# Kernel optimization log

Measured on AMD Instinct MI355X. Metric: run time of the kernel, lower is better.

## Reference

```python
import jax, jax.numpy as jnp
import numpy as np

B, L, D, H = 4, 2048, 256, 8
HD = D // H

def setup_inputs() -> dict:
    key = jax.random.key(0)
    ks = jax.random.split(key, 11)
    s = 1.0 / np.sqrt(D)
    return {
        "key": jax.random.normal(ks[0], (B, L, D), jnp.float32),
        "value": jax.random.normal(ks[1], (B, L, D), jnp.float32),
        "query": jax.random.normal(ks[2], (B, L, D), jnp.float32),
        "Wk": jax.random.normal(ks[3], (D, D), jnp.float32) * s,
        "bk": jnp.zeros((D,), jnp.float32),
        "Wq": jax.random.normal(ks[4], (D, D), jnp.float32) * s,
        "bq": jnp.zeros((D,), jnp.float32),
        "Wv": jax.random.normal(ks[5], (D, D), jnp.float32) * s,
        "bv": jnp.zeros((D,), jnp.float32),
        "Wp": jax.random.normal(ks[6], (D, D), jnp.float32) * s,
        "bp": jnp.zeros((D,), jnp.float32),
    }

def reference(key, value, query, Wk, bk, Wq, bq, Wv, bv, Wp, bp):
    # torch Linear: x @ W.T + b
    k = (key @ Wk.T + bk).reshape(B, L, H, HD).transpose(0, 2, 1, 3)   # [B,H,L,HD]
    q = (query @ Wq.T + bq).reshape(B, L, H, HD).transpose(0, 2, 1, 3)
    v = (value @ Wv.T + bv).reshape(B, L, H, HD).transpose(0, 2, 1, 3)
    att = jnp.einsum('bhqd,bhkd->bhqk', q, k) * (1.0 / np.sqrt(HD))    # [B,H,L,L]
    # causal mask (tril)
    causal = jnp.tril(jnp.ones((L, L), bool))
    att = jnp.where(causal[None, None], att, -jnp.inf)
    att = jax.nn.softmax(att, axis=-1)
    y = jnp.einsum('bhqk,bhkd->bhqd', att, v)                          # [B,H,L,HD]
    y = y.transpose(0, 2, 1, 3).reshape(B, L, D)
    return y @ Wp.T + bp
```

## Files before the change

kernel.cpp:

```cpp
#include <hip/hip_runtime.h>
#include <hip/hip_bf16.h>
#include <cstdint>

#define BB 4
#define LL 2048
#define DD 256
#define HH 8
#define HDIM 32
#define MTOT (BB * LL)
#define BHT (BB * HH)
#define XS (MTOT * DD)
#define WSZ (DD * DD)

typedef __attribute__((ext_vector_type(8))) short short8;
typedef __attribute__((ext_vector_type(4))) float f32x4;

static constexpr float SCALE = 0.17677669529663687f;
static constexpr float FMAX = 8.0f;

__device__ __forceinline__ unsigned f2bf(float f) {
    const unsigned u = __builtin_bit_cast(unsigned, f);
    return (u + 0x7fffu + ((u >> 16) & 1u)) >> 16;
}
__device__ __forceinline__ float bf2f(unsigned h) {
    return __builtin_bit_cast(float, h << 16);
}

__device__ __forceinline__ void split_store(const float4 f, unsigned short* hb,
                                            unsigned short* lb, size_t base) {
    const float fv[4] = {f.x, f.y, f.z, f.w};
    unsigned h[4], l[4];
#pragma unroll
    for (int j = 0; j < 4; ++j) {
        h[j] = f2bf(fv[j]);
        l[j] = f2bf(fv[j] - bf2f(h[j]));
    }
    *(uint2*)&hb[base] = make_uint2(h[0] | (h[1] << 16), h[2] | (h[3] << 16));
    *(uint2*)&lb[base] = make_uint2(l[0] | (l[1] << 16), l[2] | (l[3] << 16));
}

__global__ __launch_bounds__(256) void prep_x(const float* __restrict__ s0,
                                              const float* __restrict__ s1,
                                              const float* __restrict__ s2,
                                              unsigned short* __restrict__ xh,
                                              unsigned short* __restrict__ xl) {
    const int t = blockIdx.y;
    const float* src = (t == 0) ? s0 : (t == 1 ? s1 : s2);
    const size_t i4 = (size_t)blockIdx.x * 256 + threadIdx.x;
    const float4 f = ((const float4*)src)[i4];
    split_store(f, xh, xl, (size_t)t * XS + i4 * 4);
}

__global__ __launch_bounds__(256) void prep_w(const float* __restrict__ w0,
                                              const float* __restrict__ w1,
                                              const float* __restrict__ w2,
                                              const float* __restrict__ w3,
                                              unsigned short* __restrict__ wh,
                                              unsigned short* __restrict__ wl) {
    const int t = blockIdx.y;
    const float* src = (t == 0) ? w0 : (t == 1 ? w1 : (t == 2 ? w2 : w3));
    const size_t i4 = (size_t)blockIdx.x * 256 + threadIdx.x;
    const float4 f = ((const float4*)src)[i4];
    split_store(f, wh, wl, (size_t)t * WSZ + i4 * 4);
}

template <int MODE>
__global__ __launch_bounds__(256) void gemm_bf16x2(const unsigned short* __restrict__ Ah,
                                                   const unsigned short* __restrict__ Al,
                                                   const unsigned short* __restrict__ Wh,
                                                   const unsigned short* __restrict__ Wl,
                                                   const float* __restrict__ bias,
                                                   void* __restrict__ Cout) {
    const int tid = threadIdx.x;
    const int w = tid >> 6;
    const int lane = tid & 63;
    const int g = lane >> 4;
    const int c = lane & 15;
    const int bm = blockIdx.x * 64;
    const int bn = blockIdx.y * 64;
    const int m0w = bm + w * 16;

    f32x4 acc[4] = {};

    const unsigned short* arow_h = Ah + (size_t)(m0w + c) * DD + 8 * g;
    const unsigned short* arow_l = Al + (size_t)(m0w + c) * DD + 8 * g;

#pragma unroll
    for (int k0 = 0; k0 < DD; k0 += 32) {
        const short8 ah = *(const short8*)(arow_h + k0);
        const short8 al = *(const short8*)(arow_l + k0);
#pragma unroll
        for (int nf = 0; nf < 4; ++nf) {
            const size_t woff = (size_t)(bn + nf * 16 + c) * DD + k0 + 8 * g;
            const short8 wh = *(const short8*)(Wh + woff);
            const short8 wl = *(const short8*)(Wl + woff);
            acc[nf] = __builtin_amdgcn_mfma_f32_16x16x32_bf16(ah, wh, acc[nf], 0, 0, 0);
            acc[nf] = __builtin_amdgcn_mfma_f32_16x16x32_bf16(ah, wl, acc[nf], 0, 0, 0);
            acc[nf] = __builtin_amdgcn_mfma_f32_16x16x32_bf16(al, wh, acc[nf], 0, 0, 0);
        }
    }

#pragma unroll
    for (int nf = 0; nf < 4; ++nf) {
        const int n = bn + nf * 16 + c;
        const float bj = bias[n];
        if constexpr (MODE == 0) {
            float* C = (float*)Cout;
#pragma unroll
            for (int r = 0; r < 4; ++r)
                C[(size_t)(m0w + 4 * g + r) * DD + n] = acc[nf][r] + bj;
        } else if constexpr (MODE == 1 || MODE == 2) {
            unsigned short* C = (unsigned short*)Cout;
            const int h_ = n >> 5, d_ = n & 31;
#pragma unroll
            for (int r = 0; r < 4; ++r) {
                const int m = m0w + 4 * g + r;
                const int b_ = m >> 11, l_ = m & (LL - 1);
                float v = acc[nf][r] + bj;
                if (MODE == 1) v *= SCALE;
                C[(((size_t)b_ * HH + h_) * LL + l_) * HDIM + d_] = (unsigned short)f2bf(v);
            }
        } else {
            unsigned short* C = (unsigned short*)Cout;
            const int h_ = n >> 5, d_ = n & 31;
            const int m = m0w + 4 * g;
            const int b_ = m >> 11, l_ = m & (LL - 1);
            const unsigned lo = f2bf(acc[nf][0] + bj) | (f2bf(acc[nf][1] + bj) << 16);
            const unsigned hi = f2bf(acc[nf][2] + bj) | (f2bf(acc[nf][3] + bj) << 16);
            *(uint2*)&C[(((size_t)b_ * HH + h_) * HDIM + d_) * LL + l_] = make_uint2(lo, hi);
        }
    }
}

__global__ __launch_bounds__(256) void attn_mfma(const unsigned short* __restrict__ qb,
                                                 const unsigned short* __restrict__ kb,
                                                 const unsigned short* __restrict__ vt,
                                                 unsigned short* __restrict__ yh,
                                                 unsigned short* __restrict__ yl) {
    __shared__ unsigned short plds[4][16][66];
    const int tid = threadIdx.x;
    const int w = tid >> 6;
    const int lane = tid & 63;
    const int g = lane >> 4;
    const int c = lane & 15;
    const int qblk = (int)(gridDim.x - 1 - blockIdx.x);
    const int bh = blockIdx.y;
    const int qrow0 = qblk * 64 + w * 16;

    const unsigned short* Qp = qb + (size_t)bh * LL * HDIM;
    const unsigned short* Kp = kb + (size_t)bh * LL * HDIM;
    const unsigned short* Vp = vt + (size_t)bh * HDIM * LL;

    const short8 qf = *(const short8*)(Qp + (size_t)(qrow0 + c) * HDIM + g * 8);

    f32x4 y0 = {0.f, 0.f, 0.f, 0.f};
    f32x4 y1 = {0.f, 0.f, 0.f, 0.f};
    float lsum = 0.f;

    auto step = [&](int kt, bool masked) {
        const f32x4 z = {0.f, 0.f, 0.f, 0.f};
        f32x4 st[4];
#pragma unroll
        for (int t = 0; t < 4; ++t) {
            const short8 kf = *(const short8*)(Kp + (size_t)(kt + 16 * t + c) * HDIM + g * 8);
            st[t] = __builtin_amdgcn_mfma_f32_16x16x32_bf16(kf, qf, z, 0, 0, 0);
        }
        if (masked) {
#pragma unroll
            for (int t = 0; t < 4; ++t)
#pragma unroll
                for (int r = 0; r < 4; ++r)
                    if (kt + 16 * t + 4 * g + r > qrow0 + c) st[t][r] = -1e30f;
        }
#pragma unroll
        for (int t = 0; t < 4; ++t) {
            const float p0 = __expf(st[t][0] - FMAX);
            const float p1 = __expf(st[t][1] - FMAX);
            const float p2 = __expf(st[t][2] - FMAX);
            const float p3 = __expf(st[t][3] - FMAX);
            lsum += (p0 + p1) + (p2 + p3);
            const unsigned lo = f2bf(p0) | (f2bf(p1) << 16);
            const unsigned hi = f2bf(p2) | (f2bf(p3) << 16);
            *(uint2*)&plds[w][c][16 * t + 4 * g] = make_uint2(lo, hi);
        }
        asm volatile("s_waitcnt lgkmcnt(0)" ::: "memory");
        __builtin_amdgcn_sched_barrier(0);
        const unsigned short* prow = &plds[w][c][0];
        const short8 pa0 = *(const short8*)(prow + g * 8);
        const short8 pa1 = *(const short8*)(prow + 32 + g * 8);
        const short8 v00 = *(const short8*)(Vp + (size_t)c * LL + kt + g * 8);
        const short8 v10 = *(const short8*)(Vp + (size_t)c * LL + kt + 32 + g * 8);
        const short8 v01 = *(const short8*)(Vp + (size_t)(16 + c) * LL + kt + g * 8);
        const short8 v11 = *(const short8*)(Vp + (size_t)(16 + c) * LL + kt + 32 + g * 8);
        y0 = __builtin_amdgcn_mfma_f32_16x16x32_bf16(pa0, v00, y0, 0, 0, 0);
        y0 = __builtin_amdgcn_mfma_f32_16x16x32_bf16(pa1, v10, y0, 0, 0, 0);
        y1 = __builtin_amdgcn_mfma_f32_16x16x32_bf16(pa0, v01, y1, 0, 0, 0);
        y1 = __builtin_amdgcn_mfma_f32_16x16x32_bf16(pa1, v11, y1, 0, 0, 0);
    };

    for (int kt = 0; kt < qblk * 64; kt += 64) step(kt, false);
    step(qblk * 64, true);

    lsum += __shfl_xor(lsum, 16);
    lsum += __shfl_xor(lsum, 32);
#pragma unroll
    for (int r = 0; r < 4; ++r) {
        const float ls = __shfl(lsum, (lane & 48) | (4 * g + r));
        const float inv = 1.f / ls;
        const size_t base =
            ((size_t)(bh >> 3) * LL + qrow0 + 4 * g + r) * DD + (bh & 7) * HDIM;
        const float v0 = y0[r] * inv;
        const float v1 = y1[r] * inv;
        const unsigned h0 = f2bf(v0), h1 = f2bf(v1);
        yh[base + c] = (unsigned short)h0;
        yl[base + c] = (unsigned short)f2bf(v0 - bf2f(h0));
        yh[base + 16 + c] = (unsigned short)h1;
        yl[base + 16 + c] = (unsigned short)f2bf(v1 - bf2f(h1));
    }
}

extern "C" void kernel_launch(void* const* d_in, const int* in_sizes, int n_in,
                              void* d_out, int out_size, void* d_ws, size_t ws_size,
                              hipStream_t stream) {
    const float* key   = (const float*)d_in[0];
    const float* value = (const float*)d_in[1];
    const float* query = (const float*)d_in[2];
    const float* Wk = (const float*)d_in[3];
    const float* bk = (const float*)d_in[4];
    const float* Wq = (const float*)d_in[5];
    const float* bq = (const float*)d_in[6];
    const float* Wv = (const float*)d_in[7];
    const float* bv = (const float*)d_in[8];
    const float* Wp = (const float*)d_in[9];
    const float* bp = (const float*)d_in[10];
    float* out = (float*)d_out;

    unsigned short* xh = (unsigned short*)d_ws;
    unsigned short* xl = xh + (size_t)3 * XS;
    unsigned short* wh = xl + (size_t)3 * XS;
    unsigned short* wl = wh + (size_t)4 * WSZ;
    unsigned short* qb = wl + (size_t)4 * WSZ;
    unsigned short* kb = qb + XS;
    unsigned short* vt = kb + XS;
    unsigned short* yh = vt + XS;
    unsigned short* yl = yh + XS;

    prep_x<<<dim3(2048, 3), 256, 0, stream>>>(key, value, query, xh, xl);
    prep_w<<<dim3(64, 4), 256, 0, stream>>>(Wk, Wq, Wv, Wp, wh, wl);

    const unsigned short* kxh = xh, *vxh = xh + XS, *qxh = xh + 2 * (size_t)XS;
    const unsigned short* kxl = xl, *vxl = xl + XS, *qxl = xl + 2 * (size_t)XS;

    const dim3 gg(MTOT / 64, DD / 64);
    gemm_bf16x2<1><<<gg, 256, 0, stream>>>(qxh, qxl, wh + WSZ, wl + WSZ, bq, qb);
    gemm_bf16x2<2><<<gg, 256, 0, stream>>>(kxh, kxl, wh, wl, bk, kb);
    gemm_bf16x2<3><<<gg, 256, 0, stream>>>(vxh, vxl, wh + 2 * (size_t)WSZ,
                                           wl + 2 * (size_t)WSZ, bv, vt);
    attn_mfma<<<dim3(LL / 64, BHT), 256, 0, stream>>>(qb, kb, vt, yh, yl);
    gemm_bf16x2<0><<<gg, 256, 0, stream>>>(yh, yl, wh + 3 * (size_t)WSZ,
                                           wl + 3 * (size_t)WSZ, bp, out);
}
```

Before: 260.4 us.

## Merge QKV projections into one launch, halve GEMM N-tile, prefetch K in attention

The three Q/K/V projection GEMMs are merged into a single launch that selects weights, bias and output layout per block from the row range. The GEMM N tile drops from 64 to 32, which doubles the block count for better occupancy and load balance but means each A row is loaded twice as often. The attention loop is rewritten as a single loop that software-prefetches the next K tile into registers, so global load latency overlaps the softmax work. Together these cut kernel launch count and hide memory latency, at the cost of more registers and redundant A reads.

```diff
diff --git a/kernel.cpp b/kernel.cpp
--- a/kernel.cpp
+++ b/kernel.cpp
@@ -64,71 +64,108 @@
     split_store(f, wh, wl, (size_t)t * WSZ + i4 * 4);
 }
 
-template <int MODE>
-__global__ __launch_bounds__(256) void gemm_bf16x2(const unsigned short* __restrict__ Ah,
-                                                   const unsigned short* __restrict__ Al,
-                                                   const unsigned short* __restrict__ Wh,
-                                                   const unsigned short* __restrict__ Wl,
-                                                   const float* __restrict__ bias,
-                                                   void* __restrict__ Cout) {
+__device__ __forceinline__ void gemm_core(const unsigned short* __restrict__ arh,
+                                          const unsigned short* __restrict__ arl,
+                                          const unsigned short* __restrict__ Wh,
+                                          const unsigned short* __restrict__ Wl,
+                                          int bn, int c, int g, f32x4 acc[2]) {
+#pragma unroll
+    for (int k0 = 0; k0 < DD; k0 += 32) {
+        const short8 ah = *(const short8*)(arh + k0);
+        const short8 al = *(const short8*)(arl + k0);
+#pragma unroll
+        for (int nf = 0; nf < 2; ++nf) {
+            const size_t woff = (size_t)(bn + nf * 16 + c) * DD + k0 + 8 * g;
+            const short8 whf = *(const short8*)(Wh + woff);
+            const short8 wlf = *(const short8*)(Wl + woff);
+            acc[nf] = __builtin_amdgcn_mfma_f32_16x16x32_bf16(ah, whf, acc[nf], 0, 0, 0);
+            acc[nf] = __builtin_amdgcn_mfma_f32_16x16x32_bf16(ah, wlf, acc[nf], 0, 0, 0);
+            acc[nf] = __builtin_amdgcn_mfma_f32_16x16x32_bf16(al, whf, acc[nf], 0, 0, 0);
+        }
+    }
+}
+
+__global__ __launch_bounds__(256) void gemm_qkv(const unsigned short* __restrict__ xh,
+                                                const unsigned short* __restrict__ xl,
+                                                const unsigned short* __restrict__ wh,
+                                                const unsigned short* __restrict__ wl,
+                                                const float* __restrict__ bk,
+                                                const float* __restrict__ bv,
+                                                const float* __restrict__ bq,
+                                                unsigned short* __restrict__ kb,
+                                                unsigned short* __restrict__ vt,
+                                                unsigned short* __restrict__ qb) {
     const int tid = threadIdx.x;
     const int w = tid >> 6;
     const int lane = tid & 63;
     const int g = lane >> 4;
     const int c = lane & 15;
     const int bm = blockIdx.x * 64;
-    const int bn = blockIdx.y * 64;
+    const int bn = blockIdx.y * 32;
+    const int tsel = bm >> 13;
     const int m0w = bm + w * 16;
 
-    f32x4 acc[4] = {};
-
-    const unsigned short* arow_h = Ah + (size_t)(m0w + c) * DD + 8 * g;
-    const unsigned short* arow_l = Al + (size_t)(m0w + c) * DD + 8 * g;
-
-#pragma unroll
-    for (int k0 = 0; k0 < DD; k0 += 32) {
-        const short8 ah = *(const short8*)(arow_h + k0);
-        const short8 al = *(const short8*)(arow_l + k0);
-#pragma unroll
-        for (int nf = 0; nf < 4; ++nf) {
-            const size_t woff = (size_t)(bn + nf * 16 + c) * DD + k0 + 8 * g;
-            const short8 wh = *(const short8*)(Wh + woff);
-            const short8 wl = *(const short8*)(Wl + woff);
-            acc[nf] = __builtin_amdgcn_mfma_f32_16x16x32_bf16(ah, wh, acc[nf], 0, 0, 0);
-            acc[nf] = __builtin_amdgcn_mfma_f32_16x16x32_bf16(ah, wl, acc[nf], 0, 0, 0);
-            acc[nf] = __builtin_amdgcn_mfma_f32_16x16x32_bf16(al, wh, acc[nf], 0, 0, 0);
-        }
-    }
-
-#pragma unroll
-    for (int nf = 0; nf < 4; ++nf) {
+    const int wsel = (tsel == 0) ? 0 : (tsel == 1 ? 2 : 1);
+    const unsigned short* Wh = wh + (size_t)wsel * WSZ;
+    const unsigned short* Wl = wl + (size_t)wsel * WSZ;
+    const float* bias = (tsel == 0) ? bk : (tsel == 1 ? bv : bq);
+
+    f32x4 acc[2] = {};
+    gemm_core(xh + (size_t)(m0w + c) * DD + 8 * g, xl + (size_t)(m0w + c) * DD + 8 * g,
+              Wh, Wl, bn, c, g, acc);
+
+    const int lm0 = (bm & 8191) + w * 16;
+#pragma unroll
+    for (int nf = 0; nf < 2; ++nf) {
         const int n = bn + nf * 16 + c;
         const float bj = bias[n];
-        if constexpr (MODE == 0) {
-            float* C = (float*)Cout;
-#pragma unroll
-            for (int r = 0; r < 4; ++r)
-                C[(size_t)(m0w + 4 * g + r) * DD + n] = acc[nf][r] + bj;
-        } else if constexpr (MODE == 1 || MODE == 2) {
-            unsigned short* C = (unsigned short*)Cout;
-            const int h_ = n >> 5, d_ = n & 31;
-#pragma unroll
-            for (int r = 0; r < 4; ++r) {
-                const int m = m0w + 4 * g + r;
-                const int b_ = m >> 11, l_ = m & (LL - 1);
-                float v = acc[nf][r] + bj;
-                if (MODE == 1) v *= SCALE;
-                C[(((size_t)b_ * HH + h_) * LL + l_) * HDIM + d_] = (unsigned short)f2bf(v);
-            }
-        } else {
-            unsigned short* C = (unsigned short*)Cout;
-            const int h_ = n >> 5, d_ = n & 31;
-            const int m = m0w + 4 * g;
+        const int h_ = n >> 5, d_ = n & 31;
+        if (tsel == 1) {
+            const int m = lm0 + 4 * g;
             const int b_ = m >> 11, l_ = m & (LL - 1);
             const unsigned lo = f2bf(acc[nf][0] + bj) | (f2bf(acc[nf][1] + bj) << 16);
             const unsigned hi = f2bf(acc[nf][2] + bj) | (f2bf(acc[nf][3] + bj) << 16);
-            *(uint2*)&C[(((size_t)b_ * HH + h_) * HDIM + d_) * LL + l_] = make_uint2(lo, hi);
+            *(uint2*)&vt[(((size_t)b_ * HH + h_) * HDIM + d_) * LL + l_] = make_uint2(lo, hi);
+        } else {
+            unsigned short* C = (tsel == 0) ? kb : qb;
+            const float sc = (tsel == 0) ? 1.0f : SCALE;
+#pragma unroll
+            for (int r = 0; r < 4; ++r) {
+                const int m = lm0 + 4 * g + r;
+                const int b_ = m >> 11, l_ = m & (LL - 1);
+                C[(((size_t)b_ * HH + h_) * LL + l_) * HDIM + d_] =
+                    (unsigned short)f2bf((acc[nf][r] + bj) * sc);
+            }
         }
+    }
+}
+
+__global__ __launch_bounds__(256) void gemm_out(const unsigned short* __restrict__ yh,
+                                                const unsigned short* __restrict__ yl,
+                                                const unsigned short* __restrict__ Wh,
+                                                const unsigned short* __restrict__ Wl,
+                                                const float* __restrict__ bias,
+                                                float* __restrict__ out) {
+    const int tid = threadIdx.x;
+    const int w = tid >> 6;
+    const int lane = tid & 63;
+    const int g = lane >> 4;
+    const int c = lane & 15;
+    const int bm = blockIdx.x * 64;
+    const int bn = blockIdx.y * 32;
+    const int m0w = bm + w * 16;
+
+    f32x4 acc[2] = {};
+    gemm_core(yh + (size_t)(m0w + c) * DD + 8 * g, yl + (size_t)(m0w + c) * DD + 8 * g,
+              Wh, Wl, bn, c, g, acc);
+
+#pragma unroll
+    for (int nf = 0; nf < 2; ++nf) {
+        const int n = bn + nf * 16 + c;
+        const float bj = bias[n];
+#pragma unroll
+        for (int r = 0; r < 4; ++r)
+            out[(size_t)(m0w + 4 * g + r) * DD + n] = acc[nf][r] + bj;
     }
 }
 
@@ -146,6 +183,7 @@
     const int qblk = (int)(gridDim.x - 1 - blockIdx.x);
     const int bh = blockIdx.y;
     const int qrow0 = qblk * 64 + w * 16;
+    const int nt = qblk + 1;
 
     const unsigned short* Qp = qb + (size_t)bh * LL * HDIM;
     const unsigned short* Kp = kb + (size_t)bh * LL * HDIM;
@@ -157,49 +195,61 @@
     f32x4 y1 = {0.f, 0.f, 0.f, 0.f};
     float lsum = 0.f;
 
-    auto step = [&](int kt, bool masked) {
+    short8 kf0 = *(const short8*)(Kp + (size_t)(c) * HDIM + g * 8);
+    short8 kf1 = *(const short8*)(Kp + (size_t)(16 + c) * HDIM + g * 8);
+    short8 kf2 = *(const short8*)(Kp + (size_t)(32 + c) * HDIM + g * 8);
+    short8 kf3 = *(const short8*)(Kp + (size_t)(48 + c) * HDIM + g * 8);
+
+    for (int t = 0; t < nt; ++t) {
+        const int kt = t * 64;
         const f32x4 z = {0.f, 0.f, 0.f, 0.f};
         f32x4 st[4];
-#pragma unroll
-        for (int t = 0; t < 4; ++t) {
-            const short8 kf = *(const short8*)(Kp + (size_t)(kt + 16 * t + c) * HDIM + g * 8);
-            st[t] = __builtin_amdgcn_mfma_f32_16x16x32_bf16(kf, qf, z, 0, 0, 0);
-        }
-        if (masked) {
-#pragma unroll
-            for (int t = 0; t < 4; ++t)
-#pragma unroll
-                for (int r = 0; r < 4; ++r)
-                    if (kt + 16 * t + 4 * g + r > qrow0 + c) st[t][r] = -1e30f;
-        }
-#pragma unroll
-        for (int t = 0; t < 4; ++t) {
-            const float p0 = __expf(st[t][0] - FMAX);
-            const float p1 = __expf(st[t][1] - FMAX);
-            const float p2 = __expf(st[t][2] - FMAX);
-            const float p3 = __expf(st[t][3] - FMAX);
-            lsum += (p0 + p1) + (p2 + p3);
-            const unsigned lo = f2bf(p0) | (f2bf(p1) << 16);
-            const unsigned hi = f2bf(p2) | (f2bf(p3) << 16);
-            *(uint2*)&plds[w][c][16 * t + 4 * g] = make_uint2(lo, hi);
-        }
-        asm volatile("s_waitcnt lgkmcnt(0)" ::: "memory");
-        __builtin_amdgcn_sched_barrier(0);
-        const unsigned short* prow = &plds[w][c][0];
-        const short8 pa0 = *(const short8*)(prow + g * 8);
-        const short8 pa1 = *(const short8*)(prow + 32 + g * 8);
+        st[0] = __builtin_amdgcn_mfma_f32_16x16x32_bf16(kf0, qf, z, 0, 0, 0);
+        st[1] = __builtin_amdgcn_mfma_f32_16x16x32_bf16(kf1, qf, z, 0, 0, 0);
+        st[2] = __builtin_amdgcn_mfma_f32_16x16x32_bf16(kf2, qf, z, 0, 0, 0);
+        st[3] = __builtin_amdgcn_mfma_f32_16x16x32_bf16(kf3, qf, z, 0, 0, 0);
+
         const short8 v00 = *(const short8*)(Vp + (size_t)c * LL + kt + g * 8);
         const short8 v10 = *(const short8*)(Vp + (size_t)c * LL + kt + 32 + g * 8);
         const short8 v01 = *(const short8*)(Vp + (size_t)(16 + c) * LL + kt + g * 8);
         const short8 v11 = *(const short8*)(Vp + (size_t)(16 + c) * LL + kt + 32 + g * 8);
+
+        const int ktn = (t + 1 < nt) ? kt + 64 : 0;
+        kf0 = *(const short8*)(Kp + (size_t)(ktn + c) * HDIM + g * 8);
+        kf1 = *(const short8*)(Kp + (size_t)(ktn + 16 + c) * HDIM + g * 8);
+        kf2 = *(const short8*)(Kp + (size_t)(ktn + 32 + c) * HDIM + g * 8);
+        kf3 = *(const short8*)(Kp + (size_t)(ktn + 48 + c) * HDIM + g * 8);
+
+        if (t == nt - 1) {
+#pragma unroll
+            for (int i = 0; i < 4; ++i)
+#pragma unroll
+                for (int r = 0; r < 4; ++r)
+                    if (kt + 16 * i + 4 * g + r > qrow0 + c) st[i][r] = -1e30f;
+        }
+
+#pragma unroll
+        for (int i = 0; i < 4; ++i) {
+            const float p0 = __expf(st[i][0] - FMAX);
+            const float p1 = __expf(st[i][1] - FMAX);
+            const float p2 = __expf(st[i][2] - FMAX);
+            const float p3 = __expf(st[i][3] - FMAX);
+            lsum += (p0 + p1) + (p2 + p3);
+            const unsigned lo = f2bf(p0) | (f2bf(p1) << 16);
+            const unsigned hi = f2bf(p2) | (f2bf(p3) << 16);
+            *(uint2*)&plds[w][c][16 * i + 4 * g] = make_uint2(lo, hi);
+        }
+        asm volatile("s_waitcnt lgkmcnt(0)" ::: "memory");
+        __builtin_amdgcn_sched_barrier(0);
+
+        const unsigned short* prow = &plds[w][c][0];
+        const short8 pa0 = *(const short8*)(prow + g * 8);
+        const short8 pa1 = *(const short8*)(prow + 32 + g * 8);
         y0 = __builtin_amdgcn_mfma_f32_16x16x32_bf16(pa0, v00, y0, 0, 0, 0);
         y0 = __builtin_amdgcn_mfma_f32_16x16x32_bf16(pa1, v10, y0, 0, 0, 0);
         y1 = __builtin_amdgcn_mfma_f32_16x16x32_bf16(pa0, v01, y1, 0, 0, 0);
         y1 = __builtin_amdgcn_mfma_f32_16x16x32_bf16(pa1, v11, y1, 0, 0, 0);
-    };
-
-    for (int kt = 0; kt < qblk * 64; kt += 64) step(kt, false);
-    step(qblk * 64, true);
+    }
 
     lsum += __shfl_xor(lsum, 16);
     lsum += __shfl_xor(lsum, 32);
@@ -248,15 +298,8 @@
     prep_x<<<dim3(2048, 3), 256, 0, stream>>>(key, value, query, xh, xl);
     prep_w<<<dim3(64, 4), 256, 0, stream>>>(Wk, Wq, Wv, Wp, wh, wl);
 
-    const unsigned short* kxh = xh, *vxh = xh + XS, *qxh = xh + 2 * (size_t)XS;
-    const unsigned short* kxl = xl, *vxl = xl + XS, *qxl = xl + 2 * (size_t)XS;
-
-    const dim3 gg(MTOT / 64, DD / 64);
-    gemm_bf16x2<1><<<gg, 256, 0, stream>>>(qxh, qxl, wh + WSZ, wl + WSZ, bq, qb);
-    gemm_bf16x2<2><<<gg, 256, 0, stream>>>(kxh, kxl, wh, wl, bk, kb);
-    gemm_bf16x2<3><<<gg, 256, 0, stream>>>(vxh, vxl, wh + 2 * (size_t)WSZ,
-                                           wl + 2 * (size_t)WSZ, bv, vt);
+    gemm_qkv<<<dim3(384, 8), 256, 0, stream>>>(xh, xl, wh, wl, bk, bv, bq, kb, vt, qb);
     attn_mfma<<<dim3(LL / 64, BHT), 256, 0, stream>>>(qb, kb, vt, yh, yl);
-    gemm_bf16x2<0><<<gg, 256, 0, stream>>>(yh, yl, wh + 3 * (size_t)WSZ,
-                                           wl + 3 * (size_t)WSZ, bp, out);
-}
+    gemm_out<<<dim3(128, 8), 256, 0, stream>>>(yh, yl, wh + 3 * (size_t)WSZ,
+                                               wl + 3 * (size_t)WSZ, bp, out);
+}
```

Result: slower. 268.6 us (+3.1%).
